# Optimization experiments

Measured on AMD Instinct MI355X. Metric: run time of the kernel, lower is better.

Reference implementation:

```python
import jax, jax.numpy as jnp
import numpy as np

N = 100000   # nodes
E = 1600000  # edges per relation (avg in-degree 16)
D = 128      # gcn_hidden (in_feat == out_feat)
R = 2        # relations: forward_edge, backward_edge


def setup_inputs() -> dict:
    key = jax.random.key(0)
    ks = jax.random.split(key, 8)
    x = jax.random.normal(ks[0], (N, D), dtype=jnp.float32)
    src_fwd = jax.random.randint(ks[1], (E,), 0, N, dtype=jnp.int32)
    dst_fwd = jax.random.randint(ks[2], (E,), 0, N, dtype=jnp.int32)
    src_bwd = jax.random.randint(ks[3], (E,), 0, N, dtype=jnp.int32)
    dst_bwd = jax.random.randint(ks[4], (E,), 0, N, dtype=jnp.int32)
    # xavier_uniform with relu gain sqrt(2)
    gain = np.sqrt(2.0)
    lim_rel = gain * np.sqrt(6.0 / (D + D))
    rel_weight = jax.random.uniform(ks[5], (R, D, D), minval=-lim_rel, maxval=lim_rel, dtype=jnp.float32)
    loop_weight = jax.random.uniform(ks[6], (D, D), minval=-lim_rel, maxval=lim_rel, dtype=jnp.float32)
    h_bias = jnp.zeros((D,), dtype=jnp.float32)
    return {
        'x': x,
        'src_fwd': src_fwd, 'dst_fwd': dst_fwd,
        'src_bwd': src_bwd, 'dst_bwd': dst_bwd,
        'rel_weight': rel_weight, 'loop_weight': loop_weight, 'h_bias': h_bias,
    }


def _rel_conv(x, src, dst, W):
    # dgl GraphConv(norm='right', weight per relation): scatter-sum src feats to
    # dst, divide by clamped in-degree, then matmul W (in_feat == out_feat so
    # order of matmul vs aggregation is mathematically equivalent).
    msg = x[src]                                            # [E, D] gather
    agg = jax.ops.segment_sum(msg, dst, num_segments=N)     # [N, D] scatter-add
    deg = jax.ops.segment_sum(jnp.ones((src.shape[0],), x.dtype), dst, num_segments=N)
    agg = agg / jnp.clip(deg, 1.0)[:, None]                 # right norm, deg clamp(min=1)
    return agg @ W                                          # [N, D]


def reference(x, src_fwd, dst_fwd, src_bwd, dst_bwd, rel_weight, loop_weight, h_bias):
    h = _rel_conv(x, src_fwd, dst_fwd, rel_weight[0])
    h = h + _rel_conv(x, src_bwd, dst_bwd, rel_weight[1])   # HeteroGraphConv sums per-relation results
    h = h + x @ loop_weight                                 # self loop
    h = h + h_bias                                          # bias
    h = jax.nn.relu(h)                                      # activation
    return h                                                # dropout is identity in eval
```

## Files before the change

kernel.cpp:

```cpp
#include <hip/hip_runtime.h>
#include <hip/hip_bf16.h>


#define DFEAT 128
#define CH2 16384
#define PSH 6
#define NBMAX 3200
#define CAPB 1536
#define NPACK 24

typedef __attribute__((ext_vector_type(8))) short short8v;
typedef __attribute__((ext_vector_type(4))) float float4v;
typedef __attribute__((ext_vector_type(2))) unsigned int u2v;
typedef __attribute__((ext_vector_type(4))) unsigned short ushort4v;

__global__ __launch_bounds__(256) void front_kernel(
        const float4v* __restrict__ x4, ushort4v* __restrict__ xb4, int n4,
        const int* __restrict__ src0, const int* __restrict__ dst0,
        const int* __restrict__ src1, const int* __restrict__ dst1,
        int* __restrict__ cursor, unsigned* __restrict__ binned,
        const float* __restrict__ wrel, const float* __restrict__ wloop,
        unsigned short* __restrict__ wb,
        int N, int E, int nbin) {
    __shared__ int cnt[NBMAX];
    __shared__ int base[NBMAX];
    int tid = threadIdx.x;
    int bid = blockIdx.x;

    if (bid < nbin) {
        for (int i = tid; i < NBMAX; i += 256) cnt[i] = 0;
        __syncthreads();
        int lo = bid * CH2, hi = min(2 * E, lo + CH2);
        for (int i = lo + tid; i < hi; i += 256) {
            int r = (i >= E) ? 1 : 0;
            int e = i - r * E;
            int t = r ? dst1[e] : dst0[e];
            atomicAdd(&cnt[(r * N + t) >> PSH], 1);
        }
        __syncthreads();
        for (int b = tid; b < NBMAX; b += 256) {
            int c = cnt[b];
            if (c) base[b] = b * CAPB + atomicAdd(&cursor[b], c);
        }
        __syncthreads();
        for (int i = lo + tid; i < hi; i += 256) {
            int r = (i >= E) ? 1 : 0;
            int e = i - r * E;
            int s = r ? src1[e] : src0[e];
            int t = r ? dst1[e] : dst0[e];
            int p = r * N + t;
            int slot = atomicAdd(&base[p >> PSH], 1);
            binned[slot] = ((unsigned)(p & 63) << 17) | (unsigned)s;
        }
    } else if (bid < nbin + NPACK) {
        int t = (bid - nbin) * 256 + tid;
        if (t < 12 * 8 * 64) {
            int lane = t & 63;
            int kbase = (t >> 9) * 32 + (lane >> 4) * 8;
            int col = (((t >> 6) & 7) << 4) + (lane & 15);
            unsigned short tmp[8];
#pragma unroll
            for (int j = 0; j < 8; ++j) {
                int k = kbase + j;
                float v = (k < 256) ? wrel[k * DFEAT + col]
                                    : wloop[(k - 256) * DFEAT + col];
                tmp[j] = __hip_bfloat16_raw(__float2bfloat16(v)).x;
            }
            *(ushort4*)(wb + t * 8)     = make_ushort4(tmp[0], tmp[1], tmp[2], tmp[3]);
            *(ushort4*)(wb + t * 8 + 4) = make_ushort4(tmp[4], tmp[5], tmp[6], tmp[7]);
        }
    } else {
        int cb = bid - nbin - NPACK;
        int i = cb * 256 + tid;
        if (i < n4) {
            float4v v = __builtin_nontemporal_load(x4 + i);
            ushort4v o;
            o[0] = __hip_bfloat16_raw(__float2bfloat16(v[0])).x;
            o[1] = __hip_bfloat16_raw(__float2bfloat16(v[1])).x;
            o[2] = __hip_bfloat16_raw(__float2bfloat16(v[2])).x;
            o[3] = __hip_bfloat16_raw(__float2bfloat16(v[3])).x;
            xb4[i] = o;
        }
    }
}

#define CONSUME(Q0, Q1, Q2, Q3) {                                              \
    a[0] += __uint_as_float(Q0[0] << 16) + __uint_as_float(Q1[0] << 16)        \
          + __uint_as_float(Q2[0] << 16) + __uint_as_float(Q3[0] << 16);       \
    a[1] += __uint_as_float(Q0[0] & 0xffff0000u) + __uint_as_float(Q1[0] & 0xffff0000u) \
          + __uint_as_float(Q2[0] & 0xffff0000u) + __uint_as_float(Q3[0] & 0xffff0000u); \
    a[2] += __uint_as_float(Q0[1] << 16) + __uint_as_float(Q1[1] << 16)        \
          + __uint_as_float(Q2[1] << 16) + __uint_as_float(Q3[1] << 16);       \
    a[3] += __uint_as_float(Q0[1] & 0xffff0000u) + __uint_as_float(Q1[1] & 0xffff0000u) \
          + __uint_as_float(Q2[1] & 0xffff0000u) + __uint_as_float(Q3[1] & 0xffff0000u); }

__global__ __launch_bounds__(128) void agg_kernel(
        const u2v* __restrict__ xb2,
        const unsigned* __restrict__ binned,
        const int* __restrict__ cursor,
        unsigned short* __restrict__ aggb, int N, int M) {
    __shared__ unsigned ebuf[CAPB];
    __shared__ int cnt[64], cur[64], rs[64];
    int tid = threadIdx.x;
    int b = blockIdx.x;
    int total = min(cursor[b], CAPB);
    const unsigned* seg = binned + (size_t)b * CAPB;
    int P0 = b << PSH;
    int hw = tid >> 5, lane = tid & 31;

    if (tid < 64) cnt[tid] = 0;
    __syncthreads();
    for (int i = tid; i < total; i += 128)
        atomicAdd(&cnt[seg[i] >> 17], 1);
    __syncthreads();
    if (tid < 64) {
        int c = cnt[tid];
        int inc = c;
#pragma unroll
        for (int off = 1; off < 64; off <<= 1) {
            int t2 = __shfl_up(inc, off);
            if (tid >= off) inc += t2;
        }
        rs[tid] = inc - c;
        cur[tid] = inc - c;
    }
    __syncthreads();
    for (int i = tid; i < total; i += 128) {
        unsigned v = seg[i];
        int slot = atomicAdd(&cur[v >> 17], 1);
        ebuf[slot] = v & 0x1FFFFu;
    }
    __syncthreads();

    for (int pi = 0; pi < 16; ++pi) {
        int pl = hw * 16 + pi;
        int s0 = rs[pl], c = cnt[pl];
        float4v a = (float4v){0.f, 0.f, 0.f, 0.f};
        int e = 0;
        if (c >= 8) {
            u2v A0 = xb2[(size_t)ebuf[s0]     * 32 + lane];
            u2v B0 = xb2[(size_t)ebuf[s0 + 1] * 32 + lane];
            u2v C0 = xb2[(size_t)ebuf[s0 + 2] * 32 + lane];
            u2v D0 = xb2[(size_t)ebuf[s0 + 3] * 32 + lane];
            u2v A1 = xb2[(size_t)ebuf[s0 + 4] * 32 + lane];
            u2v B1 = xb2[(size_t)ebuf[s0 + 5] * 32 + lane];
            u2v C1 = xb2[(size_t)ebuf[s0 + 6] * 32 + lane];
            u2v D1 = xb2[(size_t)ebuf[s0 + 7] * 32 + lane];
            for (e = 8; e + 4 <= c; e += 4) {
                u2v nA = xb2[(size_t)ebuf[s0 + e]     * 32 + lane];
                u2v nB = xb2[(size_t)ebuf[s0 + e + 1] * 32 + lane];
                u2v nC = xb2[(size_t)ebuf[s0 + e + 2] * 32 + lane];
                u2v nD = xb2[(size_t)ebuf[s0 + e + 3] * 32 + lane];
                CONSUME(A0, B0, C0, D0);
                A0 = A1; B0 = B1; C0 = C1; D0 = D1;
                A1 = nA; B1 = nB; C1 = nC; D1 = nD;
            }
            CONSUME(A0, B0, C0, D0);
            CONSUME(A1, B1, C1, D1);
        } else if (c >= 4) {
            u2v A0 = xb2[(size_t)ebuf[s0]     * 32 + lane];
            u2v B0 = xb2[(size_t)ebuf[s0 + 1] * 32 + lane];
            u2v C0 = xb2[(size_t)ebuf[s0 + 2] * 32 + lane];
            u2v D0 = xb2[(size_t)ebuf[s0 + 3] * 32 + lane];
            CONSUME(A0, B0, C0, D0);
            e = 4;
        }
        for (; e < c; ++e) {
            int s = ebuf[s0 + e];
            u2v g = xb2[(size_t)s * 32 + lane];
            a[0] += __uint_as_float(g[0] << 16);
            a[1] += __uint_as_float(g[0] & 0xffff0000u);
            a[2] += __uint_as_float(g[1] << 16);
            a[3] += __uint_as_float(g[1] & 0xffff0000u);
        }
        int pg = P0 + pl;
        if (pg < M) {
            float inv = 1.0f / (float)max(c, 1);
            ushort4v w;
            w[0] = __hip_bfloat16_raw(__float2bfloat16(a[0] * inv)).x;
            w[1] = __hip_bfloat16_raw(__float2bfloat16(a[1] * inv)).x;
            w[2] = __hip_bfloat16_raw(__float2bfloat16(a[2] * inv)).x;
            w[3] = __hip_bfloat16_raw(__float2bfloat16(a[3] * inv)).x;
            __builtin_nontemporal_store(
                w, (ushort4v*)(aggb + (size_t)pg * DFEAT + 4 * lane));
        }
    }
}

__global__ __launch_bounds__(256) void mfma_gemm_kernel(
        const unsigned short* __restrict__ aggb,
        const unsigned short* __restrict__ xb,
        const unsigned short* __restrict__ wb,
        const float* __restrict__ bias,
        float* __restrict__ out, int N) {
    int tid = threadIdx.x;
    int wv = tid >> 6, lane = tid & 63;
    int R0 = blockIdx.x * 128 + wv * 32;
    int mrow = lane & 15, quad = lane >> 4;

    float4v acc[2][8];
#pragma unroll
    for (int rt = 0; rt < 2; ++rt)
#pragma unroll
        for (int ct = 0; ct < 8; ++ct) acc[rt][ct] = (float4v){0.f, 0.f, 0.f, 0.f};

    int n0 = min(R0 + mrow, N - 1);
    int n1 = min(R0 + 16 + mrow, N - 1);

#pragma unroll
    for (int kc = 0; kc < 12; ++kc) {
        int off = (kc & 3) * 32 + quad * 8;
        const unsigned short* s0;
        const unsigned short* s1;
        if (kc < 4)      { s0 = aggb + (size_t)n0 * DFEAT;       s1 = aggb + (size_t)n1 * DFEAT; }
        else if (kc < 8) { s0 = aggb + (size_t)(N + n0) * DFEAT; s1 = aggb + (size_t)(N + n1) * DFEAT; }
        else             { s0 = xb + (size_t)n0 * DFEAT;         s1 = xb + (size_t)n1 * DFEAT; }
        short8v a0 = *(const short8v*)(s0 + off);
        short8v a1 = *(const short8v*)(s1 + off);
#pragma unroll
        for (int ct = 0; ct < 8; ++ct) {
            short8v bfr = *(const short8v*)(wb + (((kc * 8 + ct) << 6) + lane) * 8);
            acc[0][ct] = __builtin_amdgcn_mfma_f32_16x16x32_bf16(a0, bfr, acc[0][ct], 0, 0, 0);
            acc[1][ct] = __builtin_amdgcn_mfma_f32_16x16x32_bf16(a1, bfr, acc[1][ct], 0, 0, 0);
        }
    }

#pragma unroll
    for (int ct = 0; ct < 8; ++ct) {
        int col = ct * 16 + mrow;
        float bv = bias[col];
#pragma unroll
        for (int rt = 0; rt < 2; ++rt) {
#pragma unroll
            for (int i = 0; i < 4; ++i) {
                int row = R0 + rt * 16 + quad * 4 + i;
                if (row < N)
                    __builtin_nontemporal_store(fmaxf(acc[rt][ct][i] + bv, 0.f),
                                                out + (size_t)row * DFEAT + col);
            }
        }
    }
}

extern "C" void kernel_launch(void* const* d_in, const int* in_sizes, int n_in,
                              void* d_out, int out_size, void* d_ws, size_t ws_size,
                              hipStream_t stream) {
    const float* x      = (const float*)d_in[0];
    const int* src_fwd  = (const int*)d_in[1];
    const int* dst_fwd  = (const int*)d_in[2];
    const int* src_bwd  = (const int*)d_in[3];
    const int* dst_bwd  = (const int*)d_in[4];
    const float* wrel   = (const float*)d_in[5];
    const float* wloop  = (const float*)d_in[6];
    const float* hbias  = (const float*)d_in[7];
    float* out          = (float*)d_out;

    int N = in_sizes[0] / DFEAT;
    int E = in_sizes[1];
    int M = 2 * N;
    int TE = 2 * E;
    int NB = (M + 63) / 64;

    unsigned short* wb   = (unsigned short*)d_ws;
    unsigned* binned     = (unsigned*)(wb + 12 * 8 * 64 * 8);
    unsigned short* xb   = (unsigned short*)(binned + (size_t)NB * CAPB);
    unsigned short* aggb = xb + (size_t)(N + 1) * DFEAT;
    int* cursor          = (int*)(aggb + (size_t)M * DFEAT);

    int n4 = N * (DFEAT / 4);
    int nconv = (n4 + 255) / 256;
    int nbin = (TE + CH2 - 1) / CH2;

    (void)hipMemsetAsync(cursor, 0, NB * sizeof(int), stream);

    front_kernel<<<nbin + NPACK + nconv, 256, 0, stream>>>(
        (const float4v*)x, (ushort4v*)xb, n4,
        src_fwd, dst_fwd, src_bwd, dst_bwd,
        cursor, binned, wrel, wloop, wb, N, E, nbin);

    agg_kernel<<<NB, 128, 0, stream>>>(
        (const u2v*)xb, binned, cursor, aggb, N, M);

    mfma_gemm_kernel<<<(N + 127) / 128, 256, 0, stream>>>(
        aggb, xb, wb, hbias, out, N);
}
```

Measured before the change: 365.4 us.

## Shrink binning chunks, pack LDS counters, batch edge loads, coarsen bf16 conversion

The edge-binning blocks now each process a smaller chunk (4096 instead of 16384 edges), so more blocks work in parallel. Each block keeps its per-bin counts as packed 16-bit halves in shared memory, halving the counter array and its zeroing cost. Both binning passes load four edges per thread before issuing their atomics, to get more loads in flight. The x-to-bf16 conversion blocks each handle four times as many elements. The price is about four times as many global cursor atomics, and 16-bit counters limit each bin to 65535 edges per chunk.

```diff
diff --git a/kernel.cpp b/kernel.cpp
--- a/kernel.cpp
+++ b/kernel.cpp
@@ -3,7 +3,7 @@
 
 
 #define DFEAT 128
-#define CH2 16384
+#define CH2 4096
 #define PSH 6
 #define NBMAX 3200
 #define CAPB 1536
@@ -22,35 +22,57 @@
         const float* __restrict__ wrel, const float* __restrict__ wloop,
         unsigned short* __restrict__ wb,
         int N, int E, int nbin) {
-    __shared__ int cnt[NBMAX];
+    __shared__ unsigned cntp[NBMAX / 2];
     __shared__ int base[NBMAX];
     int tid = threadIdx.x;
     int bid = blockIdx.x;
 
     if (bid < nbin) {
-        for (int i = tid; i < NBMAX; i += 256) cnt[i] = 0;
-        __syncthreads();
-        int lo = bid * CH2, hi = min(2 * E, lo + CH2);
-        for (int i = lo + tid; i < hi; i += 256) {
+        auto ldp = [&](int i) {
             int r = (i >= E) ? 1 : 0;
             int e = i - r * E;
             int t = r ? dst1[e] : dst0[e];
-            atomicAdd(&cnt[(r * N + t) >> PSH], 1);
+            return r * N + t;
+        };
+        auto lds_ = [&](int i) {
+            int r = (i >= E) ? 1 : 0;
+            int e = i - r * E;
+            return r ? src1[e] : src0[e];
+        };
+        for (int i = tid; i < NBMAX / 2; i += 256) cntp[i] = 0;
+        __syncthreads();
+        int lo = bid * CH2, hi = min(2 * E, lo + CH2);
+        for (int ii = lo + tid; ii < hi; ii += 1024) {
+            int p0 = ldp(ii);
+            int p1 = (ii + 256 < hi) ? ldp(ii + 256) : -1;
+            int p2 = (ii + 512 < hi) ? ldp(ii + 512) : -1;
+            int p3 = (ii + 768 < hi) ? ldp(ii + 768) : -1;
+            int b0 = p0 >> PSH;
+            atomicAdd(&cntp[b0 >> 1], (b0 & 1) ? 0x10000u : 1u);
+            if (p1 >= 0) { int b1 = p1 >> PSH; atomicAdd(&cntp[b1 >> 1], (b1 & 1) ? 0x10000u : 1u); }
+            if (p2 >= 0) { int b2 = p2 >> PSH; atomicAdd(&cntp[b2 >> 1], (b2 & 1) ? 0x10000u : 1u); }
+            if (p3 >= 0) { int b3 = p3 >> PSH; atomicAdd(&cntp[b3 >> 1], (b3 & 1) ? 0x10000u : 1u); }
         }
         __syncthreads();
         for (int b = tid; b < NBMAX; b += 256) {
-            int c = cnt[b];
+            int c = (int)((cntp[b >> 1] >> ((b & 1) * 16)) & 0xFFFFu);
             if (c) base[b] = b * CAPB + atomicAdd(&cursor[b], c);
         }
         __syncthreads();
-        for (int i = lo + tid; i < hi; i += 256) {
-            int r = (i >= E) ? 1 : 0;
-            int e = i - r * E;
-            int s = r ? src1[e] : src0[e];
-            int t = r ? dst1[e] : dst0[e];
-            int p = r * N + t;
-            int slot = atomicAdd(&base[p >> PSH], 1);
-            binned[slot] = ((unsigned)(p & 63) << 17) | (unsigned)s;
+        for (int ii = lo + tid; ii < hi; ii += 1024) {
+            int p0 = ldp(ii);             int s0 = lds_(ii);
+            int i1 = ii + 256, i2 = ii + 512, i3 = ii + 768;
+            int p1 = (i1 < hi) ? ldp(i1) : -1;  int s1 = (i1 < hi) ? lds_(i1) : 0;
+            int p2 = (i2 < hi) ? ldp(i2) : -1;  int s2 = (i2 < hi) ? lds_(i2) : 0;
+            int p3 = (i3 < hi) ? ldp(i3) : -1;  int s3 = (i3 < hi) ? lds_(i3) : 0;
+            { int slot = atomicAdd(&base[p0 >> PSH], 1);
+              binned[slot] = ((unsigned)(p0 & 63) << 17) | (unsigned)s0; }
+            if (p1 >= 0) { int slot = atomicAdd(&base[p1 >> PSH], 1);
+                           binned[slot] = ((unsigned)(p1 & 63) << 17) | (unsigned)s1; }
+            if (p2 >= 0) { int slot = atomicAdd(&base[p2 >> PSH], 1);
+                           binned[slot] = ((unsigned)(p2 & 63) << 17) | (unsigned)s2; }
+            if (p3 >= 0) { int slot = atomicAdd(&base[p3 >> PSH], 1);
+                           binned[slot] = ((unsigned)(p3 & 63) << 17) | (unsigned)s3; }
         }
     } else if (bid < nbin + NPACK) {
         int t = (bid - nbin) * 256 + tid;
@@ -71,15 +93,18 @@
         }
     } else {
         int cb = bid - nbin - NPACK;
-        int i = cb * 256 + tid;
-        if (i < n4) {
-            float4v v = __builtin_nontemporal_load(x4 + i);
-            ushort4v o;
-            o[0] = __hip_bfloat16_raw(__float2bfloat16(v[0])).x;
-            o[1] = __hip_bfloat16_raw(__float2bfloat16(v[1])).x;
-            o[2] = __hip_bfloat16_raw(__float2bfloat16(v[2])).x;
-            o[3] = __hip_bfloat16_raw(__float2bfloat16(v[3])).x;
-            xb4[i] = o;
+#pragma unroll
+        for (int k = 0; k < 4; ++k) {
+            int i = cb * 1024 + k * 256 + tid;
+            if (i < n4) {
+                float4v v = __builtin_nontemporal_load(x4 + i);
+                ushort4v o;
+                o[0] = __hip_bfloat16_raw(__float2bfloat16(v[0])).x;
+                o[1] = __hip_bfloat16_raw(__float2bfloat16(v[1])).x;
+                o[2] = __hip_bfloat16_raw(__float2bfloat16(v[2])).x;
+                o[3] = __hip_bfloat16_raw(__float2bfloat16(v[3])).x;
+                xb4[i] = o;
+            }
         }
     }
 }
@@ -268,7 +293,7 @@
     int* cursor          = (int*)(aggb + (size_t)M * DFEAT);
 
     int n4 = N * (DFEAT / 4);
-    int nconv = (n4 + 255) / 256;
+    int nconv = (n4 + 1023) / 1024;
     int nbin = (TE + CH2 - 1) / CH2;
 
     (void)hipMemsetAsync(cursor, 0, NB * sizeof(int), stream);
```

After: 345.6 us. -5.4%, faster.

## Replace shared-memory two-pass binning with direct global atomic slot claims

Applied to the files above, without the earlier changes.

The binning blocks no longer count per-bin occurrences in LDS and reserve ranges with one global atomic per bin. Instead each edge claims its own slot with a global atomicAdd on the bin cursor, and each thread handles four edges per iteration to overlap the index loads. The chunk size drops so more blocks run, and the bf16 conversion blocks now each process four float4 vectors per thread. This removes the LDS passes and barriers but adds 3.2M contended global atomics, plus a new CAPB bounds check that silently drops overflowing edges.

```diff
diff --git a/kernel.cpp b/kernel.cpp
--- a/kernel.cpp
+++ b/kernel.cpp
@@ -3,9 +3,8 @@
 
 
 #define DFEAT 128
-#define CH2 16384
+#define CH2 2048
 #define PSH 6
-#define NBMAX 3200
 #define CAPB 1536
 #define NPACK 24
 
@@ -22,35 +21,35 @@
         const float* __restrict__ wrel, const float* __restrict__ wloop,
         unsigned short* __restrict__ wb,
         int N, int E, int nbin) {
-    __shared__ int cnt[NBMAX];
-    __shared__ int base[NBMAX];
     int tid = threadIdx.x;
     int bid = blockIdx.x;
 
     if (bid < nbin) {
-        for (int i = tid; i < NBMAX; i += 256) cnt[i] = 0;
-        __syncthreads();
         int lo = bid * CH2, hi = min(2 * E, lo + CH2);
-        for (int i = lo + tid; i < hi; i += 256) {
-            int r = (i >= E) ? 1 : 0;
-            int e = i - r * E;
-            int t = r ? dst1[e] : dst0[e];
-            atomicAdd(&cnt[(r * N + t) >> PSH], 1);
-        }
-        __syncthreads();
-        for (int b = tid; b < NBMAX; b += 256) {
-            int c = cnt[b];
-            if (c) base[b] = b * CAPB + atomicAdd(&cursor[b], c);
-        }
-        __syncthreads();
-        for (int i = lo + tid; i < hi; i += 256) {
-            int r = (i >= E) ? 1 : 0;
-            int e = i - r * E;
-            int s = r ? src1[e] : src0[e];
-            int t = r ? dst1[e] : dst0[e];
-            int p = r * N + t;
-            int slot = atomicAdd(&base[p >> PSH], 1);
-            binned[slot] = ((unsigned)(p & 63) << 17) | (unsigned)s;
+        for (int ii = lo + tid; ii < hi; ii += 1024) {
+            int i1 = ii + 256, i2 = ii + 512, i3 = ii + 768;
+            int r0 = (ii >= E), e0 = ii - r0 * E;
+            int p0 = (r0 ? dst1[e0] : dst0[e0]) + r0 * N;
+            int s0 = r0 ? src1[e0] : src0[e0];
+            int p1 = -1, s1 = 0, p2 = -1, s2 = 0, p3 = -1, s3 = 0;
+            if (i1 < hi) { int r = (i1 >= E), e = i1 - r * E;
+                           p1 = (r ? dst1[e] : dst0[e]) + r * N; s1 = r ? src1[e] : src0[e]; }
+            if (i2 < hi) { int r = (i2 >= E), e = i2 - r * E;
+                           p2 = (r ? dst1[e] : dst0[e]) + r * N; s2 = r ? src1[e] : src0[e]; }
+            if (i3 < hi) { int r = (i3 >= E), e = i3 - r * E;
+                           p3 = (r ? dst1[e] : dst0[e]) + r * N; s3 = r ? src1[e] : src0[e]; }
+            { int b = p0 >> PSH; int slot = atomicAdd(&cursor[b], 1);
+              if (slot < CAPB) binned[(size_t)b * CAPB + slot] =
+                  ((unsigned)(p0 & 63) << 17) | (unsigned)s0; }
+            if (p1 >= 0) { int b = p1 >> PSH; int slot = atomicAdd(&cursor[b], 1);
+              if (slot < CAPB) binned[(size_t)b * CAPB + slot] =
+                  ((unsigned)(p1 & 63) << 17) | (unsigned)s1; }
+            if (p2 >= 0) { int b = p2 >> PSH; int slot = atomicAdd(&cursor[b], 1);
+              if (slot < CAPB) binned[(size_t)b * CAPB + slot] =
+                  ((unsigned)(p2 & 63) << 17) | (unsigned)s2; }
+            if (p3 >= 0) { int b = p3 >> PSH; int slot = atomicAdd(&cursor[b], 1);
+              if (slot < CAPB) binned[(size_t)b * CAPB + slot] =
+                  ((unsigned)(p3 & 63) << 17) | (unsigned)s3; }
         }
     } else if (bid < nbin + NPACK) {
         int t = (bid - nbin) * 256 + tid;
@@ -71,15 +70,18 @@
         }
     } else {
         int cb = bid - nbin - NPACK;
-        int i = cb * 256 + tid;
-        if (i < n4) {
-            float4v v = __builtin_nontemporal_load(x4 + i);
-            ushort4v o;
-            o[0] = __hip_bfloat16_raw(__float2bfloat16(v[0])).x;
-            o[1] = __hip_bfloat16_raw(__float2bfloat16(v[1])).x;
-            o[2] = __hip_bfloat16_raw(__float2bfloat16(v[2])).x;
-            o[3] = __hip_bfloat16_raw(__float2bfloat16(v[3])).x;
-            xb4[i] = o;
+#pragma unroll
+        for (int k = 0; k < 4; ++k) {
+            int i = cb * 1024 + k * 256 + tid;
+            if (i < n4) {
+                float4v v = __builtin_nontemporal_load(x4 + i);
+                ushort4v o;
+                o[0] = __hip_bfloat16_raw(__float2bfloat16(v[0])).x;
+                o[1] = __hip_bfloat16_raw(__float2bfloat16(v[1])).x;
+                o[2] = __hip_bfloat16_raw(__float2bfloat16(v[2])).x;
+                o[3] = __hip_bfloat16_raw(__float2bfloat16(v[3])).x;
+                xb4[i] = o;
+            }
         }
     }
 }
@@ -268,7 +270,7 @@
     int* cursor          = (int*)(aggb + (size_t)M * DFEAT);
 
     int n4 = N * (DFEAT / 4);
-    int nconv = (n4 + 255) / 256;
+    int nconv = (n4 + 1023) / 1024;
     int nbin = (TE + CH2 - 1) / CH2;
 
     (void)hipMemsetAsync(cursor, 0, NB * sizeof(int), stream);
```

After: 635.8 us. 1.74x slower.
